# Kernel tuning notes

Measured on AMD Instinct MI355X. Metric: run time of the kernel, lower is better.

## Reference

```python
import jax, jax.numpy as jnp
import numpy as np

N = 50000      # nodes
E = 640000     # edges
HID = 64       # hid_dim (per-head channels C)
HEADS = 4
D = HID * HEADS  # 256, conv output dim (concat=True)
LN_EPS = 1e-5


def setup_inputs() -> dict:
    key = jax.random.key(0)
    ks = jax.random.split(key, 10)
    def w(k, shape, scale=0.05):
        return jax.random.normal(k, shape, dtype=jnp.float32) * scale
    x = jax.random.normal(ks[0], (N, HID), dtype=jnp.float32)
    edge_index = jax.random.randint(ks[1], (2, E), 0, N)
    return {
        'x': x,
        'edge_index': edge_index,
        'Wq': w(ks[2], (D, HID)), 'bq': jnp.zeros((D,), jnp.float32),
        'Wk': w(ks[3], (D, HID)), 'bk': jnp.zeros((D,), jnp.float32),
        'Wv': w(ks[4], (D, HID)), 'bv': jnp.zeros((D,), jnp.float32),
        'Wskip': w(ks[5], (D, HID)), 'bskip': jnp.zeros((D,), jnp.float32),
        'Wbeta': w(ks[6], (1, 3 * D)),
        'ln_g': jnp.ones((D,), jnp.float32), 'ln_b': jnp.zeros((D,), jnp.float32),
        'Wproj': w(ks[7], (HID, D)), 'bproj': jnp.zeros((HID,), jnp.float32),
    }


def _layer(x, edge_index, Wq, bq, Wk, bk, Wv, bv, Wskip, bskip, Wbeta, ln_g, ln_b, Wproj, bproj):
    src, dst = edge_index[0], edge_index[1]  # message flows src -> dst
    # q/k/v projections, [N, H, C]
    q = (x @ Wq.T + bq).reshape(N, HEADS, HID)
    k = (x @ Wk.T + bk).reshape(N, HEADS, HID)
    v = (x @ Wv.T + bv).reshape(N, HEADS, HID)
    # edge-wise attention logits: [E, H]
    alpha = jnp.einsum('ehc,ehc->eh', q[dst], k[src]) / jnp.sqrt(jnp.float32(HID))
    # per-destination-node softmax (segment softmax)
    m = jax.ops.segment_max(alpha, dst, num_segments=N)          # [N, H]
    ex = jnp.exp(alpha - m[dst])                                 # [E, H]
    s = jax.ops.segment_sum(ex, dst, num_segments=N)             # [N, H]
    attn = ex / (s[dst] + 1e-16)                                 # [E, H]
    # weighted scatter-aggregate of values -> [N, H*C]
    msg = (v[src] * attn[..., None]).reshape(E, D)
    out = jax.ops.segment_sum(msg, dst, num_segments=N)          # [N, D]
    # beta gated skip (TransformerConv beta=True, root_weight=True)
    x_r = x @ Wskip.T + bskip                                    # [N, D]
    beta = jax.nn.sigmoid(jnp.concatenate([out, x_r, out - x_r], axis=-1) @ Wbeta.T)  # [N, 1]
    h = beta * x_r + (1.0 - beta) * out
    # LayerNorm over last dim
    mu = jnp.mean(h, axis=-1, keepdims=True)
    var = jnp.var(h, axis=-1, keepdims=True)
    h = (h - mu) * jax.lax.rsqrt(var + LN_EPS) * ln_g + ln_b
    # projection + residual + ReLU (dropout = identity in eval)
    h = h @ Wproj.T + bproj
    return jax.nn.relu(h + x)


def reference(x, edge_index, Wq, bq, Wk, bk, Wv, bv, Wskip, bskip, Wbeta, ln_g, ln_b, Wproj, bproj):
    return _layer(x, edge_index, Wq, bq, Wk, bk, Wv, bv, Wskip, bskip, Wbeta, ln_g, ln_b, Wproj, bproj)
```

## Files before the change

kernel.cpp:

```cpp
#include <hip/hip_runtime.h>
#include <stdint.h>

#define NND 50000
#define NED 640000

typedef unsigned short u16;
typedef unsigned int u32;
typedef __attribute__((ext_vector_type(8))) short short8;
typedef __attribute__((ext_vector_type(4))) float f32x4;
typedef __attribute__((ext_vector_type(2))) float fx2;

__device__ __forceinline__ float bf2f(u16 u) {
    union { u32 i; float f; } x; x.i = ((u32)u) << 16; return x.f;
}
__device__ __forceinline__ u16 f2bf(float f) {
    union { u32 i; float f; } x; x.f = f;
    u32 u = x.i;
    return (u16)((u + 0x7fffu + ((u >> 16) & 1u)) >> 16);
}
__device__ __forceinline__ float bflo(u32 w) {
    union { u32 i; float f; } x; x.i = w << 16; return x.f;
}
__device__ __forceinline__ float bfhi(u32 w) {
    union { u32 i; float f; } x; x.i = w & 0xffff0000u; return x.f;
}
__device__ __forceinline__ u32 pk2(float lo, float hi) {
    return (u32)f2bf(lo) | ((u32)f2bf(hi) << 16);
}
__device__ __forceinline__ u32 pk_fp8_4(u32 w0, u32 w1) {
    u32 p = __builtin_amdgcn_cvt_pk_fp8_f32(bflo(w0), bfhi(w0), 0, false);
    p = __builtin_amdgcn_cvt_pk_fp8_f32(bflo(w1), bfhi(w1), p, true);
    return p;
}
__device__ __forceinline__ void dec8v(u32 a, u32 b, fx2* f) {
    f[0] = __builtin_amdgcn_cvt_pk_f32_fp8(a, false);
    f[1] = __builtin_amdgcn_cvt_pk_f32_fp8(a, true);
    f[2] = __builtin_amdgcn_cvt_pk_f32_fp8(b, false);
    f[3] = __builtin_amdgcn_cvt_pk_f32_fp8(b, true);
}

#define WT_BLKS 324
#define CNT_BLKS 2500
__global__ void k_fillwt(const int* __restrict__ esrc, const int* __restrict__ edst,
                         int* __restrict__ deg, int* __restrict__ csr,
                         const float* __restrict__ Wq, const float* __restrict__ Wk,
                         const float* __restrict__ Wv, const float* __restrict__ Ws,
                         const float* __restrict__ Wp,
                         const float* __restrict__ bq, const float* __restrict__ bk,
                         const float* __restrict__ bv, const float* __restrict__ bs,
                         u16* __restrict__ wb, float* __restrict__ bias_c,
                         u16* __restrict__ wpA) {
    if (blockIdx.x >= WT_BLKS) {
        int e = (blockIdx.x - WT_BLKS) * 256 + threadIdx.x;
        if (e < NED) {
            int d = edst[e];
            int pos = atomicAdd(&deg[d], 1);
            if (pos < 64) csr[(d << 6) + pos] = esrc[e];
        }
        return;
    }
    int idx = blockIdx.x * 256 + threadIdx.x;
    if (idx < 65536) {
        int j = idx & 7;
        int lane = (idx >> 3) & 63;
        int q = (idx >> 9) & 1;
        int dt = idx >> 10;
        int dim = dt * 16 + (lane & 15);
        int k = q * 32 + ((lane >> 4) & 3) * 8 + j;
        int mat = dim >> 8, r = dim & 255;
        const float* W = (mat == 0) ? Wq : (mat == 1) ? Wk : (mat == 2) ? Wv : Ws;
        float v = W[r * 64 + k] * ((mat == 0) ? 0.125f : 1.0f);
        wb[idx] = f2bf(v);
    } else if (idx < 65536 + 1024) {
        int dim = idx - 65536;
        int mat = dim >> 8, r = dim & 255;
        const float* B = (mat == 0) ? bq : (mat == 1) ? bk : (mat == 2) ? bv : bs;
        bias_c[dim] = B[r] * ((mat == 0) ? 0.125f : 1.0f);
    } else if (idx < 65536 + 1024 + 16384) {
        int w = idx - 66560;
        int j = w & 7;
        int lane = (w >> 3) & 63;
        int kc = (w >> 9) & 7;
        int mt = w >> 12;
        int dim = mt * 16 + (lane & 15);
        int k = kc * 32 + ((lane >> 4) & 3) * 8 + j;
        wpA[w] = f2bf(Wp[dim * 256 + k]);
    }
}

#define PPAD 1040
__global__ __launch_bounds__(256) void k_proj(
    const float* __restrict__ x, const u16* __restrict__ wb,
    const float* __restrict__ bias_c,
    uint2* __restrict__ q8, uint4* __restrict__ kv8, u16* __restrict__ xr16)
{
    __shared__ u16 hb[16 * PPAD];
    const int t = threadIdx.x;
    const int wave = t >> 6, lane = t & 63;
    const int node0 = blockIdx.x * 16;
    const int lr = lane & 15, quad = lane >> 4;

    int node = node0 + lr;
    if (node > NND - 1) node = NND - 1;
    short8 xf0, xf1;
    {
        const float* xp = x + (size_t)node * 64 + quad * 8;
        float4 a = *reinterpret_cast<const float4*>(xp);
        float4 b = *reinterpret_cast<const float4*>(xp + 4);
        float4 c = *reinterpret_cast<const float4*>(xp + 32);
        float4 d = *reinterpret_cast<const float4*>(xp + 36);
        xf0[0] = (short)f2bf(a.x); xf0[1] = (short)f2bf(a.y);
        xf0[2] = (short)f2bf(a.z); xf0[3] = (short)f2bf(a.w);
        xf0[4] = (short)f2bf(b.x); xf0[5] = (short)f2bf(b.y);
        xf0[6] = (short)f2bf(b.z); xf0[7] = (short)f2bf(b.w);
        xf1[0] = (short)f2bf(c.x); xf1[1] = (short)f2bf(c.y);
        xf1[2] = (short)f2bf(c.z); xf1[3] = (short)f2bf(c.w);
        xf1[4] = (short)f2bf(d.x); xf1[5] = (short)f2bf(d.y);
        xf1[6] = (short)f2bf(d.z); xf1[7] = (short)f2bf(d.w);
    }
    #pragma unroll 4
    for (int dtl = 0; dtl < 16; ++dtl) {
        int dt = wave * 16 + dtl;
        const u16* wp = wb + (size_t)(dt * 2) * 512 + lane * 8;
        short8 a0 = *reinterpret_cast<const short8*>(wp);
        short8 a1 = *reinterpret_cast<const short8*>(wp + 512);
        f32x4 bias = *reinterpret_cast<const f32x4*>(bias_c + dt * 16 + quad * 4);
        f32x4 acc = {0.f, 0.f, 0.f, 0.f};
        acc = __builtin_amdgcn_mfma_f32_16x16x32_bf16(a0, xf0, acc, 0, 0, 0);
        acc = __builtin_amdgcn_mfma_f32_16x16x32_bf16(a1, xf1, acc, 0, 0, 0);
        uint2 st;
        st.x = pk2(acc[0] + bias[0], acc[1] + bias[1]);
        st.y = pk2(acc[2] + bias[2], acc[3] + bias[3]);
        *reinterpret_cast<uint2*>(&hb[lr * PPAD + dt * 16 + quad * 4]) = st;
    }
    __syncthreads();
    #pragma unroll
    for (int it = 0; it < 2; ++it) {
        int idx = it * 256 + t;
        int nip = idx >> 5, g = idx & 31;
        int gnode = node0 + nip;
        if (gnode < NND) {
            const u16* hp = &hb[nip * PPAD];
            *reinterpret_cast<uint4*>(xr16 + (size_t)gnode * 256 + g * 8) =
                *reinterpret_cast<const uint4*>(hp + 768 + g * 8);
            uint4 qw = *reinterpret_cast<const uint4*>(hp + g * 8);
            uint2 qs;
            qs.x = pk_fp8_4(qw.x, qw.y);
            qs.y = pk_fp8_4(qw.z, qw.w);
            q8[(size_t)gnode * 32 + g] = qs;
            uint4 kw = *reinterpret_cast<const uint4*>(hp + 256 + g * 8);
            uint4 vw = *reinterpret_cast<const uint4*>(hp + 512 + g * 8);
            uint4 kvs;
            kvs.x = pk_fp8_4(kw.x, kw.y);
            kvs.y = pk_fp8_4(kw.z, kw.w);
            kvs.z = pk_fp8_4(vw.x, vw.y);
            kvs.w = pk_fp8_4(vw.z, vw.w);
            kv8[(size_t)gnode * 32 + g] = kvs;
        }
    }
}

#define PS 264
__global__ __launch_bounds__(256) void k_attnepi(
    const int* __restrict__ deg, const int* __restrict__ csr,
    const uint2* __restrict__ q8, const uint4* __restrict__ kv8,
    const u16* __restrict__ xr16, const float* __restrict__ x,
    const float* __restrict__ Wbeta, const float* __restrict__ ln_g,
    const float* __restrict__ ln_b, const u16* __restrict__ wpA,
    const float* __restrict__ bproj, float* __restrict__ y)
{
    __shared__ u16 hn[16 * PS];
    const int t = threadIdx.x;
    const int wave = t >> 6, lane = t & 63;
    const int l32 = lane & 31, half = lane >> 5;
    const int lr = lane & 15, grp = lane >> 4;
    const int base = blockIdx.x * 16;

    for (int nt = 0; nt < 4; ++nt) {
        int lid = wave * 4 + nt;
        int node = base + lid;
        if (node >= NND) break;
        uint2 qv = q8[(size_t)node * 32 + l32];
        fx2 q[4];
        dec8v(qv.x, qv.y, q);
        int r0 = node << 6;
        int r1 = r0 + __builtin_amdgcn_readfirstlane(deg[node]);
        float s = 0.f;
        fx2 acc0 = {0.f, 0.f}, acc1 = {0.f, 0.f}, acc2 = {0.f, 0.f}, acc3 = {0.f, 0.f};
        int i = r0;
        for (; i + 8 <= r1; i += 8) {
            int c0 = csr[i + 0], c1 = csr[i + 1], c2 = csr[i + 2], c3 = csr[i + 3];
            int c4 = csr[i + 4], c5 = csr[i + 5], c6 = csr[i + 6], c7 = csr[i + 7];
            int e0 = half ? c4 : c0;
            int e1 = half ? c5 : c1;
            int e2 = half ? c6 : c2;
            int e3 = half ? c7 : c3;
            uint4 kv0 = kv8[(size_t)e0 * 32 + l32];
            uint4 kv1 = kv8[(size_t)e1 * 32 + l32];
            uint4 kv2 = kv8[(size_t)e2 * 32 + l32];
            uint4 kv3 = kv8[(size_t)e3 * 32 + l32];
            fx2 k0[4], k1[4], k2[4], k3[4];
            dec8v(kv0.x, kv0.y, k0); dec8v(kv1.x, kv1.y, k1);
            dec8v(kv2.x, kv2.y, k2); dec8v(kv3.x, kv3.y, k3);
            fx2 t0 = q[0]*k0[0] + q[1]*k0[1] + q[2]*k0[2] + q[3]*k0[3];
            fx2 t1 = q[0]*k1[0] + q[1]*k1[1] + q[2]*k1[2] + q[3]*k1[3];
            fx2 t2 = q[0]*k2[0] + q[1]*k2[1] + q[2]*k2[2] + q[3]*k2[3];
            fx2 t3 = q[0]*k3[0] + q[1]*k3[1] + q[2]*k3[2] + q[3]*k3[3];
            float pa = t0.x + t0.y, pb = t1.x + t1.y, pc = t2.x + t2.y, pd = t3.x + t3.y;
            pa += __shfl_xor(pa, 1); pa += __shfl_xor(pa, 2); pa += __shfl_xor(pa, 4);
            pb += __shfl_xor(pb, 1); pb += __shfl_xor(pb, 2); pb += __shfl_xor(pb, 4);
            pc += __shfl_xor(pc, 1); pc += __shfl_xor(pc, 2); pc += __shfl_xor(pc, 4);
            pd += __shfl_xor(pd, 1); pd += __shfl_xor(pd, 2); pd += __shfl_xor(pd, 4);
            float ea = __expf(pa), eb = __expf(pb), ec = __expf(pc), ed = __expf(pd);
            s += (ea + eb) + (ec + ed);
            fx2 ev0 = {ea, ea}, ev1 = {eb, eb}, ev2 = {ec, ec}, ev3 = {ed, ed};
            fx2 v0[4], v1[4], v2[4], v3[4];
            dec8v(kv0.z, kv0.w, v0); dec8v(kv1.z, kv1.w, v1);
            dec8v(kv2.z, kv2.w, v2); dec8v(kv3.z, kv3.w, v3);
            acc0 = acc0 + ev0*v0[0] + ev1*v1[0] + ev2*v2[0] + ev3*v3[0];
            acc1 = acc1 + ev0*v0[1] + ev1*v1[1] + ev2*v2[1] + ev3*v3[1];
            acc2 = acc2 + ev0*v0[2] + ev1*v1[2] + ev2*v2[2] + ev3*v3[2];
            acc3 = acc3 + ev0*v0[3] + ev1*v1[3] + ev2*v2[3] + ev3*v3[3];
        }
        for (; i + 4 <= r1; i += 4) {
            int c0 = csr[i + 0], c1 = csr[i + 1], c2 = csr[i + 2], c3 = csr[i + 3];
            int e0 = half ? c2 : c0;
            int e1 = half ? c3 : c1;
            uint4 kv0 = kv8[(size_t)e0 * 32 + l32];
            uint4 kv1 = kv8[(size_t)e1 * 32 + l32];
            fx2 k0[4], k1[4];
            dec8v(kv0.x, kv0.y, k0); dec8v(kv1.x, kv1.y, k1);
            fx2 t0 = q[0]*k0[0] + q[1]*k0[1] + q[2]*k0[2] + q[3]*k0[3];
            fx2 t1 = q[0]*k1[0] + q[1]*k1[1] + q[2]*k1[2] + q[3]*k1[3];
            float pa = t0.x + t0.y, pb = t1.x + t1.y;
            pa += __shfl_xor(pa, 1); pa += __shfl_xor(pa, 2); pa += __shfl_xor(pa, 4);
            pb += __shfl_xor(pb, 1); pb += __shfl_xor(pb, 2); pb += __shfl_xor(pb, 4);
            float ea = __expf(pa), eb = __expf(pb);
            s += ea + eb;
            fx2 ev0 = {ea, ea}, ev1 = {eb, eb};
            fx2 v0[4], v1[4];
            dec8v(kv0.z, kv0.w, v0); dec8v(kv1.z, kv1.w, v1);
            acc0 = acc0 + ev0*v0[0] + ev1*v1[0];
            acc1 = acc1 + ev0*v0[1] + ev1*v1[1];
            acc2 = acc2 + ev0*v0[2] + ev1*v1[2];
            acc3 = acc3 + ev0*v0[3] + ev1*v1[3];
        }
        for (; i < r1; i += 2) {
            int ii = i + half;
            bool valid = ii < r1;
            if (ii > r1 - 1) ii = r1 - 1;
            int e0 = csr[ii];
            uint4 kv0 = kv8[(size_t)e0 * 32 + l32];
            fx2 k0[4];
            dec8v(kv0.x, kv0.y, k0);
            fx2 t0 = q[0]*k0[0] + q[1]*k0[1] + q[2]*k0[2] + q[3]*k0[3];
            float pa = t0.x + t0.y;
            pa += __shfl_xor(pa, 1); pa += __shfl_xor(pa, 2); pa += __shfl_xor(pa, 4);
            float ea = valid ? __expf(pa) : 0.f;
            s += ea;
            fx2 ev0 = {ea, ea};
            fx2 v0[4];
            dec8v(kv0.z, kv0.w, v0);
            acc0 = acc0 + ev0*v0[0];
            acc1 = acc1 + ev0*v0[1];
            acc2 = acc2 + ev0*v0[2];
            acc3 = acc3 + ev0*v0[3];
        }
        float a0 = acc0.x, a1 = acc0.y, a2 = acc1.x, a3 = acc1.y;
        float a4 = acc2.x, a5 = acc2.y, a6 = acc3.x, a7 = acc3.y;
        s  += __shfl_xor(s, 32);
        a0 += __shfl_xor(a0, 32); a1 += __shfl_xor(a1, 32);
        a2 += __shfl_xor(a2, 32); a3 += __shfl_xor(a3, 32);
        a4 += __shfl_xor(a4, 32); a5 += __shfl_xor(a5, 32);
        a6 += __shfl_xor(a6, 32); a7 += __shfl_xor(a7, 32);
        float inv = 1.0f / (s + 1e-16f);
        if (half == 0) {
            uint4 st;
            st.x = pk2(a0 * inv, a1 * inv);
            st.y = pk2(a2 * inv, a3 * inv);
            st.z = pk2(a4 * inv, a5 * inv);
            st.w = pk2(a6 * inv, a7 * inv);
            *reinterpret_cast<uint4*>(&hn[lid * PS + l32 * 8]) = st;
        }
    }
    __syncthreads();

    {
        const float4* wb4 = reinterpret_cast<const float4*>(Wbeta);
        const float4* g44 = reinterpret_cast<const float4*>(ln_g);
        const float4* b44 = reinterpret_cast<const float4*>(ln_b);
        float wo[16], wx[16], wd[16], gg[16], bb[16];
        #pragma unroll
        for (int j = 0; j < 4; ++j) {
            float4 a = wb4[lr * 4 + j];
            float4 b = wb4[64 + lr * 4 + j];
            float4 c = wb4[128 + lr * 4 + j];
            float4 g = g44[lr * 4 + j];
            float4 bl = b44[lr * 4 + j];
            wo[j*4+0]=a.x; wo[j*4+1]=a.y; wo[j*4+2]=a.z; wo[j*4+3]=a.w;
            wx[j*4+0]=b.x; wx[j*4+1]=b.y; wx[j*4+2]=b.z; wx[j*4+3]=b.w;
            wd[j*4+0]=c.x; wd[j*4+1]=c.y; wd[j*4+2]=c.z; wd[j*4+3]=c.w;
            gg[j*4+0]=g.x; gg[j*4+1]=g.y; gg[j*4+2]=g.z; gg[j*4+3]=g.w;
            bb[j*4+0]=bl.x; bb[j*4+1]=bl.y; bb[j*4+2]=bl.z; bb[j*4+3]=bl.w;
        }
        int lid = wave * 4 + grp;
        int node = base + lid;
        if (node < NND) {
            uint4 u0 = *reinterpret_cast<const uint4*>(&hn[lid * PS + lr * 16]);
            uint4 u1 = *reinterpret_cast<const uint4*>(&hn[lid * PS + lr * 16 + 8]);
            const uint4* xp = reinterpret_cast<const uint4*>(xr16 + (size_t)node * 256 + lr * 16);
            uint4 v0 = xp[0], v1 = xp[1];
            float o[16], r[16];
            o[0]=bflo(u0.x); o[1]=bfhi(u0.x); o[2]=bflo(u0.y); o[3]=bfhi(u0.y);
            o[4]=bflo(u0.z); o[5]=bfhi(u0.z); o[6]=bflo(u0.w); o[7]=bfhi(u0.w);
            o[8]=bflo(u1.x); o[9]=bfhi(u1.x); o[10]=bflo(u1.y); o[11]=bfhi(u1.y);
            o[12]=bflo(u1.z); o[13]=bfhi(u1.z); o[14]=bflo(u1.w); o[15]=bfhi(u1.w);
            r[0]=bflo(v0.x); r[1]=bfhi(v0.x); r[2]=bflo(v0.y); r[3]=bfhi(v0.y);
            r[4]=bflo(v0.z); r[5]=bfhi(v0.z); r[6]=bflo(v0.w); r[7]=bfhi(v0.w);
            r[8]=bflo(v1.x); r[9]=bfhi(v1.x); r[10]=bflo(v1.y); r[11]=bfhi(v1.y);
            r[12]=bflo(v1.z); r[13]=bfhi(v1.z); r[14]=bflo(v1.w); r[15]=bfhi(v1.w);
            float part = 0.f;
            #pragma unroll
            for (int cc = 0; cc < 16; ++cc)
                part = fmaf(wo[cc], o[cc], fmaf(wx[cc], r[cc], fmaf(wd[cc], o[cc]-r[cc], part)));
            part += __shfl_xor(part, 1); part += __shfl_xor(part, 2);
            part += __shfl_xor(part, 4); part += __shfl_xor(part, 8);
            float beta = 1.0f / (1.0f + __expf(-part));
            float h[16];
            float sh = 0.f, sq = 0.f;
            #pragma unroll
            for (int cc = 0; cc < 16; ++cc) {
                h[cc] = beta * r[cc] + (1.f - beta) * o[cc];
                sh += h[cc];
                sq = fmaf(h[cc], h[cc], sq);
            }
            sh += __shfl_xor(sh, 1); sh += __shfl_xor(sh, 2);
            sh += __shfl_xor(sh, 4); sh += __shfl_xor(sh, 8);
            sq += __shfl_xor(sq, 1); sq += __shfl_xor(sq, 2);
            sq += __shfl_xor(sq, 4); sq += __shfl_xor(sq, 8);
            float mu = sh * (1.0f / 256.0f);
            float var = sq * (1.0f / 256.0f) - mu * mu;
            float ri = rsqrtf(var + 1e-5f);
            u32 pw[8];
            #pragma unroll
            for (int p = 0; p < 8; ++p) {
                float z0 = (h[p*2+0] - mu) * ri * gg[p*2+0] + bb[p*2+0];
                float z1 = (h[p*2+1] - mu) * ri * gg[p*2+1] + bb[p*2+1];
                pw[p] = pk2(z0, z1);
            }
            uint4 s0, s1;
            s0.x = pw[0]; s0.y = pw[1]; s0.z = pw[2]; s0.w = pw[3];
            s1.x = pw[4]; s1.y = pw[5]; s1.z = pw[6]; s1.w = pw[7];
            *reinterpret_cast<uint4*>(&hn[lid * PS + lr * 16]) = s0;
            *reinterpret_cast<uint4*>(&hn[lid * PS + lr * 16 + 8]) = s1;
        }
    }
    __syncthreads();

    {
        const int mt = wave;
        f32x4 acc = {0.f, 0.f, 0.f, 0.f};
        #pragma unroll
        for (int kc = 0; kc < 8; ++kc) {
            short8 a = *reinterpret_cast<const short8*>(wpA + ((size_t)(mt * 8 + kc) * 64 + lane) * 8);
            short8 b = *reinterpret_cast<const short8*>(&hn[lr * PS + kc * 32 + grp * 8]);
            acc = __builtin_amdgcn_mfma_f32_16x16x32_bf16(a, b, acc, 0, 0, 0);
        }
        int node = base + lr;
        if (node < NND) {
            int d0 = mt * 16 + grp * 4;
            float4 bp4 = *reinterpret_cast<const float4*>(bproj + d0);
            float4 xv = *reinterpret_cast<const float4*>(x + (size_t)node * 64 + d0);
            float4 rr;
            rr.x = fmaxf(acc[0] + bp4.x + xv.x, 0.f);
            rr.y = fmaxf(acc[1] + bp4.y + xv.y, 0.f);
            rr.z = fmaxf(acc[2] + bp4.z + xv.z, 0.f);
            rr.w = fmaxf(acc[3] + bp4.w + xv.w, 0.f);
            *reinterpret_cast<float4*>(y + (size_t)node * 64 + d0) = rr;
        }
    }
}

extern "C" void kernel_launch(void* const* d_in, const int* in_sizes, int n_in,
                              void* d_out, int out_size, void* d_ws, size_t ws_size,
                              hipStream_t stream) {
    const float* x     = (const float*)d_in[0];
    const int*   eidx  = (const int*)d_in[1];
    const float* Wq    = (const float*)d_in[2];
    const float* bq    = (const float*)d_in[3];
    const float* Wk    = (const float*)d_in[4];
    const float* bk    = (const float*)d_in[5];
    const float* Wv    = (const float*)d_in[6];
    const float* bv    = (const float*)d_in[7];
    const float* Wsk   = (const float*)d_in[8];
    const float* bsk   = (const float*)d_in[9];
    const float* Wbeta = (const float*)d_in[10];
    const float* lng   = (const float*)d_in[11];
    const float* lnb   = (const float*)d_in[12];
    const float* Wp    = (const float*)d_in[13];
    const float* bp    = (const float*)d_in[14];
    float* y = (float*)d_out;

    char* ws = (char*)d_ws;
    size_t off = 0;
    auto alloc = [&](size_t b) { size_t o = off; off += (b + 255) & ~(size_t)255; return o; };
    uint2* q8   = (uint2*)(ws + alloc((size_t)NND * 256));
    uint4* kv8  = (uint4*)(ws + alloc((size_t)NND * 512));
    u16*  xr16  = (u16*)(ws + alloc((size_t)NND * 512));
    int* deg    = (int*)(ws + alloc((size_t)NND * 4));
    int* csr    = (int*)(ws + alloc((size_t)NND * 64 * 4));
    u16* wb     = (u16*)(ws + alloc((size_t)65536 * 2));
    float* bias_c = (float*)(ws + alloc((size_t)1024 * 4));
    u16* wpA    = (u16*)(ws + alloc((size_t)16384 * 2));

    hipMemsetAsync(deg, 0, (size_t)NND * 4, stream);
    k_fillwt <<<WT_BLKS + CNT_BLKS, 256, 0, stream>>>(
                 eidx, eidx + NED, deg, csr,
                 Wq, Wk, Wv, Wsk, Wp, bq, bk, bv, bsk, wb, bias_c, wpA);
    k_proj   <<<(NND + 15) / 16, 256, 0, stream>>>(x, wb, bias_c, q8, kv8, xr16);
    k_attnepi<<<(NND + 15) / 16, 256, 0, stream>>>(deg, csr, q8, kv8, xr16, x,
                                                   Wbeta, lng, lnb, wpA, bp, y);
}
```

Measured before the change: 236.7 us.

## Move CSR edge fill into projection kernel so scatter overlaps node projection

```diff
diff --git a/kernel.cpp b/kernel.cpp
--- a/kernel.cpp
+++ b/kernel.cpp
@@ -39,26 +39,13 @@
     f[3] = __builtin_amdgcn_cvt_pk_f32_fp8(b, true);
 }
 
-#define WT_BLKS 324
-#define CNT_BLKS 2500
-__global__ void k_fillwt(const int* __restrict__ esrc, const int* __restrict__ edst,
-                         int* __restrict__ deg, int* __restrict__ csr,
-                         const float* __restrict__ Wq, const float* __restrict__ Wk,
-                         const float* __restrict__ Wv, const float* __restrict__ Ws,
-                         const float* __restrict__ Wp,
-                         const float* __restrict__ bq, const float* __restrict__ bk,
-                         const float* __restrict__ bv, const float* __restrict__ bs,
-                         u16* __restrict__ wb, float* __restrict__ bias_c,
-                         u16* __restrict__ wpA) {
-    if (blockIdx.x >= WT_BLKS) {
-        int e = (blockIdx.x - WT_BLKS) * 256 + threadIdx.x;
-        if (e < NED) {
-            int d = edst[e];
-            int pos = atomicAdd(&deg[d], 1);
-            if (pos < 64) csr[(d << 6) + pos] = esrc[e];
-        }
-        return;
-    }
+__global__ void k_wt(const float* __restrict__ Wq, const float* __restrict__ Wk,
+                     const float* __restrict__ Wv, const float* __restrict__ Ws,
+                     const float* __restrict__ Wp,
+                     const float* __restrict__ bq, const float* __restrict__ bk,
+                     const float* __restrict__ bv, const float* __restrict__ bs,
+                     u16* __restrict__ wb, float* __restrict__ bias_c,
+                     u16* __restrict__ wpA) {
     int idx = blockIdx.x * 256 + threadIdx.x;
     if (idx < 65536) {
         int j = idx & 7;
@@ -88,16 +75,28 @@
     }
 }
 
+#define CNT_BLKS 2500
 #define PPAD 1040
-__global__ __launch_bounds__(256) void k_proj(
+__global__ __launch_bounds__(256) void k_fillproj(
+    const int* __restrict__ esrc, const int* __restrict__ edst,
+    int* __restrict__ deg, int* __restrict__ csr,
     const float* __restrict__ x, const u16* __restrict__ wb,
     const float* __restrict__ bias_c,
     uint2* __restrict__ q8, uint4* __restrict__ kv8, u16* __restrict__ xr16)
 {
     __shared__ u16 hb[16 * PPAD];
+    if (blockIdx.x < CNT_BLKS) {
+        int e = blockIdx.x * 256 + threadIdx.x;
+        if (e < NED) {
+            int d = edst[e];
+            int pos = atomicAdd(&deg[d], 1);
+            if (pos < 64) csr[(d << 6) + pos] = esrc[e];
+        }
+        return;
+    }
     const int t = threadIdx.x;
     const int wave = t >> 6, lane = t & 63;
-    const int node0 = blockIdx.x * 16;
+    const int node0 = (blockIdx.x - CNT_BLKS) * 16;
     const int lr = lane & 15, quad = lane >> 4;
 
     int node = node0 + lr;
@@ -183,8 +182,10 @@
         uint2 qv = q8[(size_t)node * 32 + l32];
         fx2 q[4];
         dec8v(qv.x, qv.y, q);
+        int dg = __builtin_amdgcn_readfirstlane(deg[node]);
+        if (dg > 64) dg = 64;
         int r0 = node << 6;
-        int r1 = r0 + __builtin_amdgcn_readfirstlane(deg[node]);
+        int r1 = r0 + dg;
         float s = 0.f;
         fx2 acc0 = {0.f, 0.f}, acc1 = {0.f, 0.f}, acc2 = {0.f, 0.f}, acc3 = {0.f, 0.f};
         int i = r0;
@@ -343,10 +344,10 @@
             float ri = rsqrtf(var + 1e-5f);
             u32 pw[8];
             #pragma unroll
-            for (int p = 0; p < 8; ++p) {
-                float z0 = (h[p*2+0] - mu) * ri * gg[p*2+0] + bb[p*2+0];
-                float z1 = (h[p*2+1] - mu) * ri * gg[p*2+1] + bb[p*2+1];
-                pw[p] = pk2(z0, z1);
+            for (int pp = 0; pp < 8; ++pp) {
+                float z0 = (h[pp*2+0] - mu) * ri * gg[pp*2+0] + bb[pp*2+0];
+                float z1 = (h[pp*2+1] - mu) * ri * gg[pp*2+1] + bb[pp*2+1];
+                pw[pp] = pk2(z0, z1);
             }
             uint4 s0, s1;
             s0.x = pw[0]; s0.y = pw[1]; s0.z = pw[2]; s0.w = pw[3];
@@ -414,10 +415,10 @@
     u16* wpA    = (u16*)(ws + alloc((size_t)16384 * 2));
 
     hipMemsetAsync(deg, 0, (size_t)NND * 4, stream);
-    k_fillwt <<<WT_BLKS + CNT_BLKS, 256, 0, stream>>>(
-                 eidx, eidx + NED, deg, csr,
-                 Wq, Wk, Wv, Wsk, Wp, bq, bk, bv, bsk, wb, bias_c, wpA);
-    k_proj   <<<(NND + 15) / 16, 256, 0, stream>>>(x, wb, bias_c, q8, kv8, xr16);
-    k_attnepi<<<(NND + 15) / 16, 256, 0, stream>>>(deg, csr, q8, kv8, xr16, x,
-                                                   Wbeta, lng, lnb, wpA, bp, y);
-}
+    k_wt      <<<324, 256, 0, stream>>>(Wq, Wk, Wv, Wsk, Wp, bq, bk, bv, bsk,
+                                        wb, bias_c, wpA);
+    k_fillproj<<<CNT_BLKS + (NND + 15) / 16, 256, 0, stream>>>(
+                 eidx, eidx + NED, deg, csr, x, wb, bias_c, q8, kv8, xr16);
+    k_attnepi <<<(NND + 15) / 16, 256, 0, stream>>>(deg, csr, q8, kv8, xr16, x,
+                                                    Wbeta, lng, lnb, wpA, bp, y);
+}
```

Result: no change. 232.4 us (-1.8%).
